# Optimization experiments

Measured on AMD Instinct MI355X. Metric: run time of the kernel, lower is better.

Reference implementation:

```python
import jax, jax.numpy as jnp
import numpy as np

B, L, D = 32, 128, 48          # batch, time steps, features
R = 64                          # no_reference_time_point
INIT_TIME, MAX_TS = 0.0, 48.0   # linspace bounds for reference time points


def setup_inputs() -> dict:
    key = jax.random.key(0)
    ks = jax.random.split(key, 10)
    def glorot(k, shape):
        fan_in = int(np.prod(shape[:-1])) if len(shape) > 1 else shape[0]
        fan_out = shape[-1]
        lim = float(np.sqrt(6.0 / (fan_in + fan_out)))
        return jax.random.uniform(k, shape, jnp.float32, -lim, lim)
    return {
        "X": jax.random.normal(ks[0], (B, L, D), jnp.float32),
        "T": jax.random.uniform(ks[1], (B, L, D), jnp.float32) * MAX_TS,
        "M": jax.random.uniform(ks[2], (B, L, D), jnp.float32),
        "DT": jax.random.uniform(ks[3], (B, L, D), jnp.float32),
        "P": jax.random.normal(ks[4], (B, L, D), jnp.float32),
        "alpha": glorot(ks[5], (R, 1, 1)),
        "w_t": glorot(ks[6], (R, L, D, 5)),
        "b_t": glorot(ks[7], (R, L, D, 1)),
        "w_v": glorot(ks[8], (R, L, D)),
        "b_v": glorot(ks[9], (R, 1, D)),
    }


def reference(X, T, M, DT, P, alpha, w_t, b_t, w_v, b_v) -> jnp.ndarray:
    # reference time points: [R,1,1]
    ref = jnp.linspace(INIT_TIME, MAX_TS, R, dtype=jnp.float32).reshape(R, 1, 1)
    # broadcast inputs over reference axis: [B,R,L,D]
    t = T[:, None, :, :]
    dist = jnp.abs(t - ref)                         # type_distance == 'abs'
    kernel = jnp.exp(-jax.nn.relu(alpha) * dist)    # [B,R,L,D]
    x = X[:, None, :, :] * jnp.ones((1, R, 1, 1), jnp.float32)
    intensity = jax.nn.relu(x * kernel)             # [B,R,L,D]
    # stack the 5 channels: [B,R,L,D,5]
    c = jnp.stack(
        [x,
         intensity,
         jnp.broadcast_to(M[:, None, :, :], x.shape),
         jnp.broadcast_to(DT[:, None, :, :], x.shape),
         jnp.broadcast_to(P[:, None, :, :], x.shape)],
        axis=-1)
    # temporal projection: sum over channel axis (b_t broadcast over the 5 channels)
    h = jax.nn.relu(jnp.sum(w_t * c + b_t, axis=-1))       # [B,R,L,D]
    # value projection: sum over time-step axis L (b_v [R,1,D] broadcast over L)
    out = jax.nn.relu(jnp.sum(w_v * h + b_v, axis=2))       # [B,R,D]
    return out
```

## Files before the change

kernel.cpp:

```cpp
#include <hip/hip_runtime.h>

#define PB 32
#define PL 128
#define PD 48
#define PR 64

#define GLDS(gsrc, ldst)                                                      \
    __builtin_amdgcn_global_load_lds(                                         \
        (const __attribute__((address_space(1))) void*)(gsrc),                \
        (__attribute__((address_space(3))) void*)(ldst), 16, 0, 0)

__device__ __forceinline__ void compute4(
    const float4 x4, const float4 t4, const float4 m4, const float4 dt4,
    const float4 p4, const float* __restrict__ w20, const float4 bt4,
    const float4 wv4, const float ar, const float refr, float4& acc)
{
    const float xs[4]  = {x4.x,  x4.y,  x4.z,  x4.w};
    const float ts[4]  = {t4.x,  t4.y,  t4.z,  t4.w};
    const float ms[4]  = {m4.x,  m4.y,  m4.z,  m4.w};
    const float dts[4] = {dt4.x, dt4.y, dt4.z, dt4.w};
    const float ps[4]  = {p4.x,  p4.y,  p4.z,  p4.w};
    const float bts[4] = {bt4.x, bt4.y, bt4.z, bt4.w};
    const float wvs[4] = {wv4.x, wv4.y, wv4.z, wv4.w};
    float a[4] = {acc.x, acc.y, acc.z, acc.w};
    #pragma unroll
    for (int j = 0; j < 4; ++j) {
        const float x = xs[j];
        const float dist = fabsf(ts[j] - refr);
        const float kern = __expf(-ar * dist);
        float inten = x * kern;
        inten = inten > 0.0f ? inten : 0.0f;
        float h = w20[j*5 + 0] * x
                + w20[j*5 + 1] * inten
                + w20[j*5 + 2] * ms[j]
                + w20[j*5 + 3] * dts[j]
                + w20[j*5 + 4] * ps[j]
                + 5.0f * bts[j];
        h = h > 0.0f ? h : 0.0f;
        a[j] += wvs[j] * h;
    }
    acc = make_float4(a[0], a[1], a[2], a[3]);
}

__global__ __launch_bounds__(384) void alnn_kernel(
    const float* __restrict__ X,
    const float* __restrict__ T,
    const float* __restrict__ M,
    const float* __restrict__ DT,
    const float* __restrict__ P,
    const float* __restrict__ alpha,
    const float* __restrict__ w_t,
    const float* __restrict__ b_t,
    const float* __restrict__ w_v,
    const float* __restrict__ b_v,
    float* __restrict__ out)
{
    __shared__ __align__(16) float smem[15360];

    const int bid = blockIdx.x;
    const int rrb = bid & 31;
    const int bbb = bid >> 5;
    const int r0 = rrb * 2;
    const int b0 = bbb * 4;
    const int tid = threadIdx.x;
    const int lg = tid / 12;
    const int dq = tid - lg * 12;

    const float ar0 = fmaxf(alpha[r0], 0.0f);
    const float ar1 = fmaxf(alpha[r0 + 1], 0.0f);
    const float refr0 = 48.0f * (float)r0 / 63.0f;
    const float refr1 = 48.0f * (float)(r0 + 1) / 63.0f;

    int io = b0 * (PL * PD) + lg * PD + dq * 4;
    int ws = r0 * (PL * PD * 5) + tid * 4;
    int vo = r0 * (PL * PD) + lg * PD + dq * 4;

    float4 acc[4][2];
    #pragma unroll
    for (int bi = 0; bi < 4; ++bi)
        #pragma unroll
        for (int ri = 0; ri < 2; ++ri)
            acc[bi][ri] = make_float4(0.f, 0.f, 0.f, 0.f);

    const float* wl0 = smem + lg * 240 + dq * 20;
    const float* wl1 = wl0 + 7680;

    #pragma unroll 1
    for (int li = 0; li < 4; ++li) {
        __syncthreads();

        #pragma unroll
        for (int k = 0; k < 5; ++k) {
            GLDS(w_t + ws + k * 1536,          smem + tid * 4 + k * 1536);
            GLDS(w_t + ws + 30720 + k * 1536,  smem + 7680 + tid * 4 + k * 1536);
        }

        float4 x4[4], t4[4], m4[4], dt4[4], p4[4];
        #pragma unroll
        for (int bi = 0; bi < 4; ++bi) {
            const int o = io + bi * (PL * PD);
            x4[bi]  = *(const float4*)(X  + o);
            t4[bi]  = *(const float4*)(T  + o);
            m4[bi]  = *(const float4*)(M  + o);
            dt4[bi] = *(const float4*)(DT + o);
            p4[bi]  = *(const float4*)(P  + o);
        }
        const float4 bt0 = *(const float4*)(b_t + vo);
        const float4 wv0 = *(const float4*)(w_v + vo);
        const float4 bt1 = *(const float4*)(b_t + vo + PL * PD);
        const float4 wv1 = *(const float4*)(w_v + vo + PL * PD);

        __syncthreads();

        float w0[20], w1[20];
        #pragma unroll
        for (int q = 0; q < 5; ++q) {
            *(float4*)(w0 + q * 4) = *(const float4*)(wl0 + q * 4);
            *(float4*)(w1 + q * 4) = *(const float4*)(wl1 + q * 4);
        }

        #pragma unroll
        for (int bi = 0; bi < 4; ++bi) {
            compute4(x4[bi], t4[bi], m4[bi], dt4[bi], p4[bi], w0, bt0, wv0,
                     ar0, refr0, acc[bi][0]);
            compute4(x4[bi], t4[bi], m4[bi], dt4[bi], p4[bi], w1, bt1, wv1,
                     ar1, refr1, acc[bi][1]);
        }

        io += 32 * PD;
        ws += 32 * PD * 5;
        vo += 32 * PD;
    }

    __syncthreads();

    float4* part  = reinterpret_cast<float4*>(smem);
    float4* part2 = part + 32 * 97;

    #pragma unroll
    for (int bi = 0; bi < 4; ++bi)
        #pragma unroll
        for (int ri = 0; ri < 2; ++ri)
            part[lg * 97 + bi * 24 + ri * 12 + dq] = acc[bi][ri];
    __syncthreads();

    {
        const int q = tid / 96;
        const int o = tid - q * 96;
        float4 s = part[(q * 8) * 97 + o];
        #pragma unroll
        for (int g = 1; g < 8; ++g) {
            const float4 v = part[(q * 8 + g) * 97 + o];
            s.x += v.x; s.y += v.y; s.z += v.z; s.w += v.w;
        }
        part2[q * 97 + o] = s;
    }
    __syncthreads();

    if (tid < 96) {
        const int o = tid;
        const int bi = o / 24;
        const int ri = (o - bi * 24) / 12;
        const int dqo = o - bi * 24 - ri * 12;
        float4 s = part2[o];
        #pragma unroll
        for (int g = 1; g < 4; ++g) {
            const float4 v = part2[g * 97 + o];
            s.x += v.x; s.y += v.y; s.z += v.z; s.w += v.w;
        }
        const int r = r0 + ri;
        const int b = b0 + bi;
        const float4 bv4 = *(const float4*)(b_v + r * PD + dqo * 4);
        s.x = fmaxf(s.x + 128.0f * bv4.x, 0.0f);
        s.y = fmaxf(s.y + 128.0f * bv4.y, 0.0f);
        s.z = fmaxf(s.z + 128.0f * bv4.z, 0.0f);
        s.w = fmaxf(s.w + 128.0f * bv4.w, 0.0f);
        *(float4*)(out + b * (PR * PD) + r * PD + dqo * 4) = s;
    }
}

extern "C" void kernel_launch(void* const* d_in, const int* in_sizes, int n_in,
                              void* d_out, int out_size, void* d_ws, size_t ws_size,
                              hipStream_t stream) {
    const float* X     = (const float*)d_in[0];
    const float* T     = (const float*)d_in[1];
    const float* M     = (const float*)d_in[2];
    const float* DT    = (const float*)d_in[3];
    const float* P     = (const float*)d_in[4];
    const float* alpha = (const float*)d_in[5];
    const float* w_t   = (const float*)d_in[6];
    const float* b_t   = (const float*)d_in[7];
    const float* w_v   = (const float*)d_in[8];
    const float* b_v   = (const float*)d_in[9];
    float* out = (float*)d_out;

    alnn_kernel<<<256, 384, 0, stream>>>(X, T, M, DT, P, alpha, w_t, b_t, w_v, b_v, out);
}
```

Measured before the change: 97.11 us.

## Double-buffer w_t LDS loads to overlap with compute across reference halves

Loads of the w_t weight tiles into LDS are now software-pipelined instead of load-all-then-compute. The next half-tile's direct global-to-LDS transfer is issued before computing on the current half, and explicit s_waitcnt vmcnt(5) plus s_barrier replace the two __syncthreads per iteration. Since each CU runs only one block, the aim is to hide global-load latency behind the exp/FMA work. In exchange, a buffer half can be refilled while slower threads may still be reading it into registers, because no barrier separates those reads from the next overwrite, so it relies on hand-tuned wait counts.

New measurement: 93.91 us. -3.3%, faster.

```diff
diff --git a/kernel.cpp b/kernel.cpp
--- a/kernel.cpp
+++ b/kernel.cpp
@@ -72,8 +72,9 @@
     const float refr1 = 48.0f * (float)(r0 + 1) / 63.0f;
 
     int io = b0 * (PL * PD) + lg * PD + dq * 4;
-    int ws = r0 * (PL * PD * 5) + tid * 4;
     int vo = r0 * (PL * PD) + lg * PD + dq * 4;
+    int wbase = r0 * 30720;
+    const int tso = tid * 4;
 
     float4 acc[4][2];
     #pragma unroll
@@ -85,16 +86,12 @@
     const float* wl0 = smem + lg * 240 + dq * 20;
     const float* wl1 = wl0 + 7680;
 
+    #pragma unroll
+    for (int k = 0; k < 5; ++k)
+        GLDS(w_t + wbase + tso + k * 1536, smem + tso + k * 1536);
+
     #pragma unroll 1
     for (int li = 0; li < 4; ++li) {
-        __syncthreads();
-
-        #pragma unroll
-        for (int k = 0; k < 5; ++k) {
-            GLDS(w_t + ws + k * 1536,          smem + tid * 4 + k * 1536);
-            GLDS(w_t + ws + 30720 + k * 1536,  smem + 7680 + tid * 4 + k * 1536);
-        }
-
         float4 x4[4], t4[4], m4[4], dt4[4], p4[4];
         #pragma unroll
         for (int bi = 0; bi < 4; ++bi) {
@@ -110,26 +107,45 @@
         const float4 bt1 = *(const float4*)(b_t + vo + PL * PD);
         const float4 wv1 = *(const float4*)(w_v + vo + PL * PD);
 
-        __syncthreads();
-
-        float w0[20], w1[20];
-        #pragma unroll
-        for (int q = 0; q < 5; ++q) {
-            *(float4*)(w0 + q * 4) = *(const float4*)(wl0 + q * 4);
-            *(float4*)(w1 + q * 4) = *(const float4*)(wl1 + q * 4);
-        }
-
-        #pragma unroll
-        for (int bi = 0; bi < 4; ++bi) {
-            compute4(x4[bi], t4[bi], m4[bi], dt4[bi], p4[bi], w0, bt0, wv0,
-                     ar0, refr0, acc[bi][0]);
-            compute4(x4[bi], t4[bi], m4[bi], dt4[bi], p4[bi], w1, bt1, wv1,
-                     ar1, refr1, acc[bi][1]);
+        #pragma unroll
+        for (int k = 0; k < 5; ++k)
+            GLDS(w_t + wbase + 30720 + tso + k * 1536,
+                 smem + 7680 + tso + k * 1536);
+        asm volatile("s_waitcnt vmcnt(5)\n\ts_barrier" ::: "memory");
+        {
+            float w0[20];
+            #pragma unroll
+            for (int q = 0; q < 5; ++q)
+                *(float4*)(w0 + q * 4) = *(const float4*)(wl0 + q * 4);
+            #pragma unroll
+            for (int bi = 0; bi < 4; ++bi)
+                compute4(x4[bi], t4[bi], m4[bi], dt4[bi], p4[bi], w0, bt0, wv0,
+                         ar0, refr0, acc[bi][0]);
+        }
+
+        if (li < 3) {
+            #pragma unroll
+            for (int k = 0; k < 5; ++k)
+                GLDS(w_t + wbase + 7680 + tso + k * 1536,
+                     smem + tso + k * 1536);
+            asm volatile("s_waitcnt vmcnt(5)\n\ts_barrier" ::: "memory");
+        } else {
+            asm volatile("s_waitcnt vmcnt(0)\n\ts_barrier" ::: "memory");
+        }
+        {
+            float w1[20];
+            #pragma unroll
+            for (int q = 0; q < 5; ++q)
+                *(float4*)(w1 + q * 4) = *(const float4*)(wl1 + q * 4);
+            #pragma unroll
+            for (int bi = 0; bi < 4; ++bi)
+                compute4(x4[bi], t4[bi], m4[bi], dt4[bi], p4[bi], w1, bt1, wv1,
+                         ar1, refr1, acc[bi][1]);
         }
 
         io += 32 * PD;
-        ws += 32 * PD * 5;
         vo += 32 * PD;
+        wbase += 7680;
     }
 
     __syncthreads();
```
